# Kernel optimization log

Hardware: AMD Instinct MI355X
Metric: run time of the kernel (lower is better)

Reference implementation:

```python
import jax, jax.numpy as jnp
import numpy as np

EMBED, NUM_CLASSES, K, BETA = 96, 3, 3, 0.75
B, H, W = 4, 512, 512
N = H * W // 16            # 16384 sampled points
N_IMP = int(BETA * N)      # 12288 importance points
N_COV = N - N_IMP          # 4096 coverage points


def point_sample(inp, points):
    """Bilinear sample inp [B,C,H,W] at points [B,N,2] in [0,1] (x,y order).
    Matches F.grid_sample(..., mode='bilinear', padding_mode='zeros', align_corners=False)
    applied to grid = 2*points - 1."""
    Bb, C, Hh, Ww = inp.shape
    g = 2.0 * points - 1.0
    ix = ((g[..., 0] + 1.0) * Ww - 1.0) / 2.0   # [B,N]
    iy = ((g[..., 1] + 1.0) * Hh - 1.0) / 2.0
    x0 = jnp.floor(ix)
    y0 = jnp.floor(iy)
    wx1 = ix - x0
    wx0 = 1.0 - wx1
    wy1 = iy - y0
    wy0 = 1.0 - wy1
    flat = inp.reshape(Bb, C, Hh * Ww)

    def corner(xc, yc, w):
        valid = (xc >= 0) & (xc < Ww) & (yc >= 0) & (yc < Hh)
        xi = jnp.clip(xc, 0, Ww - 1).astype(jnp.int32)
        yi = jnp.clip(yc, 0, Hh - 1).astype(jnp.int32)
        idx = (yi * Ww + xi)[:, None, :]                     # [B,1,N]
        v = jnp.take_along_axis(flat, idx, axis=2)           # [B,C,N]
        return v * (w * valid.astype(w.dtype))[:, None, :]

    return (corner(x0, y0, wx0 * wy0)
            + corner(x0 + 1.0, y0, wx1 * wy0)
            + corner(x0, y0 + 1.0, wx0 * wy1)
            + corner(x0 + 1.0, y0 + 1.0, wx1 * wy1))


def setup_inputs() -> dict:
    key = jax.random.key(0)
    ks = jax.random.split(key, 6)
    x = jax.random.normal(ks[0], (B, EMBED, H, W), dtype=jnp.float32)
    res = jax.random.normal(ks[1], (B, NUM_CLASSES, H, W), dtype=jnp.float32)
    out = jax.random.normal(ks[2], (B, NUM_CLASSES, H, W), dtype=jnp.float32)
    w_mlp = jax.random.normal(ks[3], (NUM_CLASSES, EMBED + NUM_CLASSES), dtype=jnp.float32) * 0.02
    over_gen = jax.random.uniform(ks[4], (B, K * N, 2), dtype=jnp.float32)
    coverage = jax.random.uniform(ks[5], (B, N_COV, 2), dtype=jnp.float32)
    return {"x": x, "res": res, "out": out, "w_mlp": w_mlp,
            "over_gen": over_gen, "coverage": coverage}


def reference(x, res, out, w_mlp, over_gen, coverage):
    # sampling_points (training branch): uncertainty from squared error map
    mask = jnp.square(out - res)                       # [B,C,H,W]
    ms = -jnp.sort(-mask, axis=1)                      # channels sorted descending
    og_map = point_sample(ms, over_gen)                # [B,C,K*N]
    uncert = og_map[:, 1] - og_map[:, 0]               # -(top1 - top2), [B,K*N]
    _, idx = jax.lax.top_k(uncert, N_IMP)              # [B,N_IMP]
    importance = jnp.take_along_axis(over_gen, idx[..., None], axis=1)  # [B,N_IMP,2]
    points = jnp.concatenate([importance, coverage], axis=1)            # [B,N,2]

    coarse = point_sample(out, points)                 # [B,C,N]
    fine = point_sample(x, points)                     # [B,EMBED,N]
    feat = jnp.concatenate([coarse, fine], axis=1)     # [B,C+EMBED,N]
    rend = jax.nn.relu(jnp.einsum('oc,bcn->bon', w_mlp, feat))  # 1x1 Conv1d, no bias
    return rend
```

## Files before the change

kernel.cpp:

```cpp
#include <hip/hip_runtime.h>
#include <stdint.h>

#define Bb    4
#define EMBED 96
#define NCH   3
#define Hh    512
#define Ww    512
#define HWSZ  (Hh * Ww)
#define KN    49152
#define NPT   16384
#define NIMP  12288
#define NCOV  4096
#define SORTN 65536

__device__ __forceinline__ float opaque(float v) {
    asm volatile("" : "+v"(v));
    return v;
}

__device__ __forceinline__ void ref_coords(float p, int& i0, float& w0, float& w1) {
    float g  = 2.0f * p - 1.0f;
    float t  = (g + 1.0f) * 512.0f - 1.0f;
    float ix = t * 0.5f;
    float f  = floorf(ix);
    i0 = (int)f;
    w1 = ix - f;
    w0 = 1.0f - w1;
}

__device__ __forceinline__ uint32_t sortable_desc32(float v) {
    uint32_t u = __float_as_uint(v);
    uint32_t asc = (u >> 31) ? ~u : (u ^ 0x80000000u);
    return ~asc;
}

__device__ __forceinline__ uint32_t part1by1(uint32_t v) {
    v &= 0xFFFFu;
    v = (v | (v << 8)) & 0x00FF00FFu;
    v = (v | (v << 4)) & 0x0F0F0F0Fu;
    v = (v | (v << 2)) & 0x33333333u;
    v = (v | (v << 1)) & 0x55555555u;
    return v;
}

__global__ void build_maps(const float* __restrict__ res,
                           const float* __restrict__ outm,
                           float2* __restrict__ maps) {
    int lb  = blockIdx.y;
    int pix = blockIdx.x * blockDim.x + threadIdx.x;
    const float* r0 = res  + (size_t)lb * NCH * HWSZ;
    const float* o0 = outm + (size_t)lb * NCH * HWSZ;
    float d0 = opaque(o0[pix]            - r0[pix]);
    float d1 = opaque(o0[HWSZ + pix]     - r0[HWSZ + pix]);
    float d2 = opaque(o0[2 * HWSZ + pix] - r0[2 * HWSZ + pix]);
    float a  = opaque(d0 * d0);
    float bq = opaque(d1 * d1);
    float c  = opaque(d2 * d2);
    float m0 = fmaxf(fmaxf(a, bq), c);
    float m1 = fmaxf(fminf(a, bq), fminf(fmaxf(a, bq), c));
    maps[(size_t)lb * HWSZ + pix] = make_float2(m0, m1);
}

__global__ void uncert_keys_maps(const float2* __restrict__ maps,
                                 const float* __restrict__ over_gen,
                                 uint64_t* __restrict__ keys) {
    int lb = blockIdx.y;
    int i  = blockIdx.x * blockDim.x + threadIdx.x;
    if (i >= KN) { keys[(size_t)lb * SORTN + i] = 0xFFFFFFFFFFFFFFFFull; return; }

    float px = over_gen[((size_t)lb * KN + i) * 2 + 0];
    float py = over_gen[((size_t)lb * KN + i) * 2 + 1];
    int x0, y0;
    float wx0, wx1, wy0, wy1;
    ref_coords(px, x0, wx0, wx1);
    ref_coords(py, y0, wy0, wy1);

    const float2* mp = maps + (size_t)lb * HWSZ;
    int   cxs[4] = {x0, x0 + 1, x0, x0 + 1};
    int   cys[4] = {y0, y0, y0 + 1, y0 + 1};
    float wxs[4] = {wx0, wx1, wx0, wx1};
    float wys[4] = {wy0, wy0, wy1, wy1};

    float acc0 = 0.0f, acc1 = 0.0f;
#pragma unroll
    for (int q = 0; q < 4; ++q) {
        int xq = cxs[q], yq = cys[q];
        if (xq < 0 || xq >= Ww || yq < 0 || yq >= Hh) continue;
        float2 m = mp[yq * Ww + xq];
        float wq = opaque(wxs[q] * wys[q]);
        float t0 = opaque(wq * m.x);
        float t1 = opaque(wq * m.y);
        acc0 = opaque(acc0 + t0);
        acc1 = opaque(acc1 + t1);
    }
    float u = opaque(acc1 - acc0);
    keys[(size_t)lb * SORTN + i] =
        ((uint64_t)sortable_desc32(u) << 32) | (uint32_t)i;
}

__global__ void uncert_keys_direct(const float* __restrict__ res,
                                   const float* __restrict__ outm,
                                   const float* __restrict__ over_gen,
                                   uint64_t* __restrict__ keys) {
    int lb = blockIdx.y;
    int i  = blockIdx.x * blockDim.x + threadIdx.x;
    if (i >= KN) { keys[(size_t)lb * SORTN + i] = 0xFFFFFFFFFFFFFFFFull; return; }

    float px = over_gen[((size_t)lb * KN + i) * 2 + 0];
    float py = over_gen[((size_t)lb * KN + i) * 2 + 1];
    int x0, y0;
    float wx0, wx1, wy0, wy1;
    ref_coords(px, x0, wx0, wx1);
    ref_coords(py, y0, wy0, wy1);

    const float* r0 = res  + (size_t)lb * NCH * HWSZ;
    const float* o0 = outm + (size_t)lb * NCH * HWSZ;
    int   cxs[4] = {x0, x0 + 1, x0, x0 + 1};
    int   cys[4] = {y0, y0, y0 + 1, y0 + 1};
    float wxs[4] = {wx0, wx1, wx0, wx1};
    float wys[4] = {wy0, wy0, wy1, wy1};

    float acc0 = 0.0f, acc1 = 0.0f;
#pragma unroll
    for (int q = 0; q < 4; ++q) {
        int xq = cxs[q], yq = cys[q];
        if (xq < 0 || xq >= Ww || yq < 0 || yq >= Hh) continue;
        int off = yq * Ww + xq;
        float d0 = opaque(o0[off]            - r0[off]);
        float d1 = opaque(o0[HWSZ + off]     - r0[HWSZ + off]);
        float d2 = opaque(o0[2 * HWSZ + off] - r0[2 * HWSZ + off]);
        float a  = opaque(d0 * d0);
        float bq = opaque(d1 * d1);
        float c  = opaque(d2 * d2);
        float m0 = fmaxf(fmaxf(a, bq), c);
        float m1 = fmaxf(fminf(a, bq), fminf(fmaxf(a, bq), c));
        float wq = opaque(wxs[q] * wys[q]);
        float t0 = opaque(wq * m0);
        float t1 = opaque(wq * m1);
        acc0 = opaque(acc0 + t0);
        acc1 = opaque(acc1 + t1);
    }
    float u = opaque(acc1 - acc0);
    keys[(size_t)lb * SORTN + i] =
        ((uint64_t)sortable_desc32(u) << 32) | (uint32_t)i;
}

__global__ void __launch_bounds__(1024) bitonic_local_first_g(uint64_t* __restrict__ keys,
                                                              int tile_mask) {
    __shared__ uint64_t sh[2048];
    uint64_t* base = keys + (size_t)blockIdx.x * 2048;
    int t = threadIdx.x;
    sh[t]        = base[t];
    sh[t + 1024] = base[t + 1024];
    __syncthreads();
    int gbase = (blockIdx.x & tile_mask) << 11;
    for (int k = 2; k <= 2048; k <<= 1) {
        for (int j = k >> 1; j >= 1; j >>= 1) {
            int low = t & (j - 1);
            int i = ((t ^ low) << 1) | low;
            int l = i | j;
            bool up = (((gbase + i) & k) == 0);
            uint64_t a = sh[i], c = sh[l];
            if ((a > c) == up) { sh[i] = c; sh[l] = a; }
            __syncthreads();
        }
    }
    base[t]        = sh[t];
    base[t + 1024] = sh[t + 1024];
}

__global__ void bitonic_global_g(uint64_t* __restrict__ keys, int j, int k, int pbits) {
    int t = blockIdx.x * blockDim.x + threadIdx.x;
    int b = t >> pbits;
    int p = t & ((1 << pbits) - 1);
    int low = p & (j - 1);
    int i = ((p ^ low) << 1) | low;
    int l = i | j;
    bool up = ((i & k) == 0);
    uint64_t* kb = keys + ((size_t)b << (pbits + 1));
    uint64_t a = kb[i], c = kb[l];
    if ((a > c) == up) { kb[i] = c; kb[l] = a; }
}

__global__ void __launch_bounds__(1024) bitonic_local_k_g(uint64_t* __restrict__ keys,
                                                          int k, int tile_mask) {
    __shared__ uint64_t sh[2048];
    uint64_t* base = keys + (size_t)blockIdx.x * 2048;
    int t = threadIdx.x;
    sh[t]        = base[t];
    sh[t + 1024] = base[t + 1024];
    __syncthreads();
    int gbase = (blockIdx.x & tile_mask) << 11;
    bool up = ((gbase & k) == 0);
    for (int j = 1024; j >= 1; j >>= 1) {
        int low = t & (j - 1);
        int i = ((t ^ low) << 1) | low;
        int l = i | j;
        uint64_t a = sh[i], c = sh[l];
        if ((a > c) == up) { sh[i] = c; sh[l] = a; }
        __syncthreads();
    }
    base[t]        = sh[t];
    base[t + 1024] = sh[t + 1024];
}

static void run_sort_g(uint64_t* keys, int nb, int seg, hipStream_t stream) {
    int tiles = seg / 2048, tile_mask = tiles - 1;
    int pbits = 31 - __builtin_clz((unsigned)(seg >> 1));
    bitonic_local_first_g<<<nb * tiles, 1024, 0, stream>>>(keys, tile_mask);
    for (int k = 4096; k <= seg; k <<= 1) {
        for (int j = k >> 1; j >= 2048; j >>= 1)
            bitonic_global_g<<<nb * (seg / 2) / 256, 256, 0, stream>>>(keys, j, k, pbits);
        bitonic_local_k_g<<<nb * tiles, 1024, 0, stream>>>(keys, k, tile_mask);
    }
}

__global__ void pkey_kernel(const uint64_t* __restrict__ keys,
                            const float* __restrict__ over_gen,
                            const float* __restrict__ coverage,
                            uint64_t* __restrict__ pkeys) {
    int lb = blockIdx.y;
    int n  = blockIdx.x * blockDim.x + threadIdx.x;
    float px, py;
    if (n < NIMP) {
        uint32_t idx = (uint32_t)keys[((size_t)lb << 16) + n];
        if (idx >= KN) idx = 0;
        px = over_gen[((size_t)lb * KN + idx) * 2 + 0];
        py = over_gen[((size_t)lb * KN + idx) * 2 + 1];
    } else {
        int m = n - NIMP;
        px = coverage[((size_t)lb * NCOV + m) * 2 + 0];
        py = coverage[((size_t)lb * NCOV + m) * 2 + 1];
    }
    int x0, y0;
    float w0, w1;
    ref_coords(px, x0, w0, w1);
    int xi = x0;
    ref_coords(py, y0, w0, w1);
    int yi = y0;
    xi = min(max(xi, 0), Ww - 1);
    yi = min(max(yi, 0), Hh - 1);
    uint32_t morton = part1by1((uint32_t)xi) | (part1by1((uint32_t)yi) << 1);
    pkeys[(size_t)lb * NPT + n] = ((uint64_t)morton << 32) | (uint32_t)n;
}

__global__ void render_kernel(const float* __restrict__ x,
                              const float* __restrict__ outm,
                              const float* __restrict__ w_mlp,
                              const float* __restrict__ over_gen,
                              const float* __restrict__ coverage,
                              const uint64_t* __restrict__ keys,
                              const uint64_t* __restrict__ pkeys,
                              float* __restrict__ dst) {
    int gid = blockIdx.x * blockDim.x + threadIdx.x;
    int pt = gid >> 3, r = gid & 7;
    int lb = blockIdx.y;
    int n = pt;
    if (pkeys) n = (uint32_t)pkeys[(size_t)lb * NPT + pt];

    float px, py;
    if (n < NIMP) {
        uint32_t idx = (uint32_t)keys[((size_t)lb << 16) + n];
        if (idx >= KN) idx = 0;
        px = over_gen[((size_t)lb * KN + idx) * 2 + 0];
        py = over_gen[((size_t)lb * KN + idx) * 2 + 1];
    } else {
        int m = n - NIMP;
        px = coverage[((size_t)lb * NCOV + m) * 2 + 0];
        py = coverage[((size_t)lb * NCOV + m) * 2 + 1];
    }

    int x0, y0;
    float wx0, wx1, wy0, wy1;
    ref_coords(px, x0, wx0, wx1);
    ref_coords(py, y0, wy0, wy1);

    int   cxs[4] = {x0, x0 + 1, x0, x0 + 1};
    int   cys[4] = {y0, y0, y0 + 1, y0 + 1};
    float wcs[4] = {wx0 * wy0, wx1 * wy0, wx0 * wy1, wx1 * wy1};
    bool  vld[4];
#pragma unroll
    for (int q = 0; q < 4; ++q)
        vld[q] = (cxs[q] >= 0) & (cxs[q] < Ww) & (cys[q] >= 0) & (cys[q] < Hh);

    float acc0 = 0.0f, acc1 = 0.0f, acc2 = 0.0f;
    for (int c = r; c < NCH + EMBED; c += 8) {
        const float* src = (c < NCH)
            ? (outm + ((size_t)lb * NCH + c) * HWSZ)
            : (x + ((size_t)lb * EMBED + (c - NCH)) * HWSZ);
        float f = 0.0f;
#pragma unroll
        for (int q = 0; q < 4; ++q) {
            if (vld[q]) f += wcs[q] * src[cys[q] * Ww + cxs[q]];
        }
        acc0 += w_mlp[c] * f;
        acc1 += w_mlp[99 + c] * f;
        acc2 += w_mlp[198 + c] * f;
    }
#pragma unroll
    for (int d = 1; d < 8; d <<= 1) {
        acc0 += __shfl_xor(acc0, d);
        acc1 += __shfl_xor(acc1, d);
        acc2 += __shfl_xor(acc2, d);
    }
    if (r == 0) {
        size_t ob = (size_t)lb * 3 * NPT + n;
        dst[ob]           = fmaxf(acc0, 0.0f);
        dst[ob + NPT]     = fmaxf(acc1, 0.0f);
        dst[ob + 2 * NPT] = fmaxf(acc2, 0.0f);
    }
}

extern "C" void kernel_launch(void* const* d_in, const int* in_sizes, int n_in,
                              void* d_out, int out_size, void* d_ws, size_t ws_size,
                              hipStream_t stream) {
    const float* x        = (const float*)d_in[0];
    const float* res      = (const float*)d_in[1];
    const float* outm     = (const float*)d_in[2];
    const float* w_mlp    = (const float*)d_in[3];
    const float* over_gen = (const float*)d_in[4];
    const float* coverage = (const float*)d_in[5];
    float* dst = (float*)d_out;

    const size_t keys_sz = (size_t)Bb * SORTN * sizeof(uint64_t);
    const size_t pkey_sz = (size_t)Bb * NPT * sizeof(uint64_t);
    const size_t maps_sz = (size_t)Bb * HWSZ * sizeof(float2);

    uint64_t* keys = (uint64_t*)d_ws;
    dim3 gU(SORTN / 256, Bb), gP(NPT / 256, Bb), gD(NPT * 8 / 256, Bb);

    if (ws_size >= keys_sz + pkey_sz + maps_sz) {
        uint64_t* pkeys = (uint64_t*)((char*)d_ws + keys_sz);
        float2*   maps  = (float2*)((char*)d_ws + keys_sz + pkey_sz);
        dim3 gM(HWSZ / 256, Bb);
        build_maps<<<gM, 256, 0, stream>>>(res, outm, maps);
        uncert_keys_maps<<<gU, 256, 0, stream>>>(maps, over_gen, keys);
        run_sort_g(keys, Bb, SORTN, stream);
        pkey_kernel<<<gP, 256, 0, stream>>>(keys, over_gen, coverage, pkeys);
        run_sort_g(pkeys, Bb, NPT, stream);
        render_kernel<<<gD, 256, 0, stream>>>(x, outm, w_mlp, over_gen, coverage,
                                              keys, pkeys, dst);
    } else if (ws_size >= keys_sz + pkey_sz) {
        uint64_t* pkeys = (uint64_t*)((char*)d_ws + keys_sz);
        uncert_keys_direct<<<gU, 256, 0, stream>>>(res, outm, over_gen, keys);
        run_sort_g(keys, Bb, SORTN, stream);
        pkey_kernel<<<gP, 256, 0, stream>>>(keys, over_gen, coverage, pkeys);
        run_sort_g(pkeys, Bb, NPT, stream);
        render_kernel<<<gD, 256, 0, stream>>>(x, outm, w_mlp, over_gen, coverage,
                                              keys, pkeys, dst);
    } else {
        uncert_keys_direct<<<gU, 256, 0, stream>>>(res, outm, over_gen, keys);
        run_sort_g(keys, Bb, SORTN, stream);
        render_kernel<<<gD, 256, 0, stream>>>(x, outm, w_mlp, over_gen, coverage,
                                              keys, (const uint64_t*)nullptr, dst);
    }
}
```

Before: 311.1 us.

## Fuse global bitonic passes in shared memory and bucket-sort points by Morton key

The large top-k sort now runs all global-stride bitonic steps for each merge stage in one shared-memory kernel that gathers strided groups, instead of one launch per step. The second bitonic sort, which reordered sample points by Morton code for locality, is replaced with a histogram, scan and atomic scatter into 1024 coarse buckets. This cuts kernel launches and global memory passes. The cost is that point order inside a bucket depends on atomics and is not deterministic, which affects only locality, not the result.

```diff
diff --git a/kernel.cpp b/kernel.cpp
--- a/kernel.cpp
+++ b/kernel.cpp
@@ -12,6 +12,7 @@
 #define NIMP  12288
 #define NCOV  4096
 #define SORTN 65536
+#define NBUCK 1024
 
 __device__ __forceinline__ float opaque(float v) {
     asm volatile("" : "+v"(v));
@@ -145,15 +146,14 @@
         ((uint64_t)sortable_desc32(u) << 32) | (uint32_t)i;
 }
 
-__global__ void __launch_bounds__(1024) bitonic_local_first_g(uint64_t* __restrict__ keys,
-                                                              int tile_mask) {
+__global__ void __launch_bounds__(1024) bitonic_local_first(uint64_t* __restrict__ keys) {
     __shared__ uint64_t sh[2048];
     uint64_t* base = keys + (size_t)blockIdx.x * 2048;
     int t = threadIdx.x;
     sh[t]        = base[t];
     sh[t + 1024] = base[t + 1024];
     __syncthreads();
-    int gbase = (blockIdx.x & tile_mask) << 11;
+    int gbase = (blockIdx.x & 31) << 11;
     for (int k = 2; k <= 2048; k <<= 1) {
         for (int j = k >> 1; j >= 1; j >>= 1) {
             int low = t & (j - 1);
@@ -169,28 +169,55 @@
     base[t + 1024] = sh[t + 1024];
 }
 
-__global__ void bitonic_global_g(uint64_t* __restrict__ keys, int j, int k, int pbits) {
-    int t = blockIdx.x * blockDim.x + threadIdx.x;
-    int b = t >> pbits;
-    int p = t & ((1 << pbits) - 1);
-    int low = p & (j - 1);
-    int i = ((p ^ low) << 1) | low;
-    int l = i | j;
-    bool up = ((i & k) == 0);
-    uint64_t* kb = keys + ((size_t)b << (pbits + 1));
-    uint64_t a = kb[i], c = kb[l];
-    if ((a > c) == up) { kb[i] = c; kb[l] = a; }
-}
-
-__global__ void __launch_bounds__(1024) bitonic_local_k_g(uint64_t* __restrict__ keys,
-                                                          int k, int tile_mask) {
+__global__ void __launch_bounds__(1024) bitonic_global_fused(uint64_t* __restrict__ keys,
+                                                             int m) {
+    __shared__ uint64_t sh[2048];
+    int lb  = blockIdx.y;
+    int blk = blockIdx.x;
+    int t   = threadIdx.x;
+    int GS  = 1 << m;
+    int GPB = 2048 >> m;
+    int gstart = blk * GPB;
+    int esh = 11 - m;
+    uint64_t* base = keys + ((size_t)lb << 16);
+
+    for (int s = t; s < 2048; s += 1024) {
+        int e  = s >> esh;
+        int gl = s & (GPB - 1);
+        int g  = gstart + gl;
+        int full = (g & 2047) | (e << 11) | ((g >> 11) << (11 + m));
+        sh[s] = base[full];
+    }
+    __syncthreads();
+    for (int jl = GS >> 1; jl >= 1; jl >>= 1) {
+        int gl = t & (GPB - 1);
+        int pe = t >> esh;
+        int low = pe & (jl - 1);
+        int e0 = ((pe ^ low) << 1) | low;
+        int e1 = e0 | jl;
+        bool up = ((((gstart + gl) >> 11) & 1) == 0);
+        int s0 = e0 * GPB + gl, s1 = e1 * GPB + gl;
+        uint64_t a = sh[s0], c = sh[s1];
+        if ((a > c) == up) { sh[s0] = c; sh[s1] = a; }
+        __syncthreads();
+    }
+    for (int s = t; s < 2048; s += 1024) {
+        int e  = s >> esh;
+        int gl = s & (GPB - 1);
+        int g  = gstart + gl;
+        int full = (g & 2047) | (e << 11) | ((g >> 11) << (11 + m));
+        base[full] = sh[s];
+    }
+}
+
+__global__ void __launch_bounds__(1024) bitonic_local_k(uint64_t* __restrict__ keys, int k) {
     __shared__ uint64_t sh[2048];
     uint64_t* base = keys + (size_t)blockIdx.x * 2048;
     int t = threadIdx.x;
     sh[t]        = base[t];
     sh[t + 1024] = base[t + 1024];
     __syncthreads();
-    int gbase = (blockIdx.x & tile_mask) << 11;
+    int gbase = (blockIdx.x & 31) << 11;
     bool up = ((gbase & k) == 0);
     for (int j = 1024; j >= 1; j >>= 1) {
         int low = t & (j - 1);
@@ -204,21 +231,19 @@
     base[t + 1024] = sh[t + 1024];
 }
 
-static void run_sort_g(uint64_t* keys, int nb, int seg, hipStream_t stream) {
-    int tiles = seg / 2048, tile_mask = tiles - 1;
-    int pbits = 31 - __builtin_clz((unsigned)(seg >> 1));
-    bitonic_local_first_g<<<nb * tiles, 1024, 0, stream>>>(keys, tile_mask);
-    for (int k = 4096; k <= seg; k <<= 1) {
-        for (int j = k >> 1; j >= 2048; j >>= 1)
-            bitonic_global_g<<<nb * (seg / 2) / 256, 256, 0, stream>>>(keys, j, k, pbits);
-        bitonic_local_k_g<<<nb * tiles, 1024, 0, stream>>>(keys, k, tile_mask);
-    }
-}
-
-__global__ void pkey_kernel(const uint64_t* __restrict__ keys,
+static void run_sort_big(uint64_t* keys, int nb, hipStream_t stream) {
+    bitonic_local_first<<<nb * 32, 1024, 0, stream>>>(keys);
+    for (int kbit = 12; kbit <= 16; ++kbit) {
+        bitonic_global_fused<<<dim3(32, nb), 1024, 0, stream>>>(keys, kbit - 11);
+        bitonic_local_k<<<nb * 32, 1024, 0, stream>>>(keys, 1 << kbit);
+    }
+}
+
+__global__ void hist_kernel(const uint64_t* __restrict__ keys,
                             const float* __restrict__ over_gen,
                             const float* __restrict__ coverage,
-                            uint64_t* __restrict__ pkeys) {
+                            uint32_t* __restrict__ hist,
+                            uint32_t* __restrict__ mort) {
     int lb = blockIdx.y;
     int n  = blockIdx.x * blockDim.x + threadIdx.x;
     float px, py;
@@ -235,13 +260,40 @@
     int x0, y0;
     float w0, w1;
     ref_coords(px, x0, w0, w1);
-    int xi = x0;
     ref_coords(py, y0, w0, w1);
-    int yi = y0;
-    xi = min(max(xi, 0), Ww - 1);
-    yi = min(max(yi, 0), Hh - 1);
+    int xi = min(max(x0, 0), Ww - 1);
+    int yi = min(max(y0, 0), Hh - 1);
     uint32_t morton = part1by1((uint32_t)xi) | (part1by1((uint32_t)yi) << 1);
-    pkeys[(size_t)lb * NPT + n] = ((uint64_t)morton << 32) | (uint32_t)n;
+    uint32_t bucket = morton >> 8;
+    mort[(size_t)lb * NPT + n] = bucket;
+    atomicAdd(&hist[(size_t)lb * NBUCK + bucket], 1u);
+}
+
+__global__ void __launch_bounds__(1024) scan_kernel(const uint32_t* __restrict__ hist,
+                                                    uint32_t* __restrict__ offs) {
+    __shared__ uint32_t sh[NBUCK];
+    int lb = blockIdx.x;
+    int t  = threadIdx.x;
+    uint32_t orig = hist[(size_t)lb * NBUCK + t];
+    sh[t] = orig;
+    __syncthreads();
+    for (int d = 1; d < NBUCK; d <<= 1) {
+        uint32_t add = (t >= d) ? sh[t - d] : 0u;
+        __syncthreads();
+        sh[t] += add;
+        __syncthreads();
+    }
+    offs[(size_t)lb * NBUCK + t] = sh[t] - orig;
+}
+
+__global__ void scatter_kernel(const uint32_t* __restrict__ mort,
+                               uint32_t* __restrict__ offs,
+                               uint32_t* __restrict__ porder) {
+    int lb = blockIdx.y;
+    int n  = blockIdx.x * blockDim.x + threadIdx.x;
+    uint32_t b = mort[(size_t)lb * NPT + n];
+    uint32_t pos = atomicAdd(&offs[(size_t)lb * NBUCK + b], 1u);
+    porder[(size_t)lb * NPT + pos] = (uint32_t)n;
 }
 
 __global__ void render_kernel(const float* __restrict__ x,
@@ -250,13 +302,13 @@
                               const float* __restrict__ over_gen,
                               const float* __restrict__ coverage,
                               const uint64_t* __restrict__ keys,
-                              const uint64_t* __restrict__ pkeys,
+                              const uint32_t* __restrict__ porder,
                               float* __restrict__ dst) {
     int gid = blockIdx.x * blockDim.x + threadIdx.x;
     int pt = gid >> 3, r = gid & 7;
     int lb = blockIdx.y;
     int n = pt;
-    if (pkeys) n = (uint32_t)pkeys[(size_t)lb * NPT + pt];
+    if (porder) n = porder[(size_t)lb * NPT + pt];
 
     float px, py;
     if (n < NIMP) {
@@ -323,35 +375,51 @@
     float* dst = (float*)d_out;
 
     const size_t keys_sz = (size_t)Bb * SORTN * sizeof(uint64_t);
-    const size_t pkey_sz = (size_t)Bb * NPT * sizeof(uint64_t);
+    const size_t hist_sz = (size_t)Bb * NBUCK * sizeof(uint32_t);
+    const size_t offs_sz = hist_sz;
+    const size_t mort_sz = (size_t)Bb * NPT * sizeof(uint32_t);
+    const size_t pord_sz = mort_sz;
+    const size_t reor_sz = hist_sz + offs_sz + mort_sz + pord_sz;
     const size_t maps_sz = (size_t)Bb * HWSZ * sizeof(float2);
 
     uint64_t* keys = (uint64_t*)d_ws;
     dim3 gU(SORTN / 256, Bb), gP(NPT / 256, Bb), gD(NPT * 8 / 256, Bb);
 
-    if (ws_size >= keys_sz + pkey_sz + maps_sz) {
-        uint64_t* pkeys = (uint64_t*)((char*)d_ws + keys_sz);
-        float2*   maps  = (float2*)((char*)d_ws + keys_sz + pkey_sz);
+    if (ws_size >= keys_sz + reor_sz + maps_sz) {
+        char* pbase = (char*)d_ws + keys_sz;
+        uint32_t* hist   = (uint32_t*)pbase;
+        uint32_t* offs   = (uint32_t*)(pbase + hist_sz);
+        uint32_t* mort   = (uint32_t*)(pbase + hist_sz + offs_sz);
+        uint32_t* porder = (uint32_t*)(pbase + hist_sz + offs_sz + mort_sz);
+        float2*   maps   = (float2*)(pbase + reor_sz);
         dim3 gM(HWSZ / 256, Bb);
         build_maps<<<gM, 256, 0, stream>>>(res, outm, maps);
         uncert_keys_maps<<<gU, 256, 0, stream>>>(maps, over_gen, keys);
-        run_sort_g(keys, Bb, SORTN, stream);
-        pkey_kernel<<<gP, 256, 0, stream>>>(keys, over_gen, coverage, pkeys);
-        run_sort_g(pkeys, Bb, NPT, stream);
+        run_sort_big(keys, Bb, stream);
+        hipMemsetAsync(hist, 0, hist_sz, stream);
+        hist_kernel<<<gP, 256, 0, stream>>>(keys, over_gen, coverage, hist, mort);
+        scan_kernel<<<Bb, NBUCK, 0, stream>>>(hist, offs);
+        scatter_kernel<<<gP, 256, 0, stream>>>(mort, offs, porder);
         render_kernel<<<gD, 256, 0, stream>>>(x, outm, w_mlp, over_gen, coverage,
-                                              keys, pkeys, dst);
-    } else if (ws_size >= keys_sz + pkey_sz) {
-        uint64_t* pkeys = (uint64_t*)((char*)d_ws + keys_sz);
+                                              keys, porder, dst);
+    } else if (ws_size >= keys_sz + reor_sz) {
+        char* pbase = (char*)d_ws + keys_sz;
+        uint32_t* hist   = (uint32_t*)pbase;
+        uint32_t* offs   = (uint32_t*)(pbase + hist_sz);
+        uint32_t* mort   = (uint32_t*)(pbase + hist_sz + offs_sz);
+        uint32_t* porder = (uint32_t*)(pbase + hist_sz + offs_sz + mort_sz);
         uncert_keys_direct<<<gU, 256, 0, stream>>>(res, outm, over_gen, keys);
-        run_sort_g(keys, Bb, SORTN, stream);
-        pkey_kernel<<<gP, 256, 0, stream>>>(keys, over_gen, coverage, pkeys);
-        run_sort_g(pkeys, Bb, NPT, stream);
+        run_sort_big(keys, Bb, stream);
+        hipMemsetAsync(hist, 0, hist_sz, stream);
+        hist_kernel<<<gP, 256, 0, stream>>>(keys, over_gen, coverage, hist, mort);
+        scan_kernel<<<Bb, NBUCK, 0, stream>>>(hist, offs);
+        scatter_kernel<<<gP, 256, 0, stream>>>(mort, offs, porder);
         render_kernel<<<gD, 256, 0, stream>>>(x, outm, w_mlp, over_gen, coverage,
-                                              keys, pkeys, dst);
+                                              keys, porder, dst);
     } else {
         uncert_keys_direct<<<gU, 256, 0, stream>>>(res, outm, over_gen, keys);
-        run_sort_g(keys, Bb, SORTN, stream);
+        run_sort_big(keys, Bb, stream);
         render_kernel<<<gD, 256, 0, stream>>>(x, outm, w_mlp, over_gen, coverage,
-                                              keys, (const uint64_t*)nullptr, dst);
-    }
-}
+                                              keys, (const uint32_t*)nullptr, dst);
+    }
+}
```

Measured after the change: 283.8 us, median of 2. 1.1x faster.
